# Optimization experiments

Measured on AMD Instinct MI355X. Metric: run time of the kernel, lower is better.

Reference implementation:

```python
import math
import jax, jax.numpy as jnp
import numpy as np

B, S, HID = 1, 2048, 4096
NH, NKV, D = 32, 8, 128
THETA = 10000.0


def setup_inputs() -> dict:
    key = jax.random.key(0)
    k1, k2, k3, k4, k5 = jax.random.split(key, 5)
    hidden_states = jax.random.normal(k1, (B, S, HID), dtype=jnp.float32)
    k_cache = jax.random.normal(k2, (B, NKV, S, D), dtype=jnp.float32)
    v_cache = jax.random.normal(k3, (B, NKV, S, D), dtype=jnp.float32)
    Wq = jax.random.normal(k4, (HID, NH * D), dtype=jnp.float32) * 0.02
    Wo = jax.random.normal(k5, (NH * D, HID), dtype=jnp.float32) * 0.02
    position_ids = jnp.broadcast_to(jnp.arange(S, dtype=jnp.int32), (B, S))
    # causal mask: True = masked out (torch.where(mask, -10000, scores))
    attention_mask = jnp.broadcast_to(
        jnp.triu(jnp.ones((S, S), dtype=bool), k=1)[None, None], (B, 1, S, S)
    )
    return {
        "hidden_states": hidden_states,
        "k_cache": k_cache,
        "v_cache": v_cache,
        "Wq": Wq,
        "Wo": Wo,
        "position_ids": position_ids,
        "attention_mask": attention_mask,
    }


def _rotate_half(x):
    x1, x2 = jnp.split(x, 2, axis=-1)
    return jnp.concatenate([-x2, x1], axis=-1)


def _rope_tables(position_ids):
    # Llama rotary embedding gathered at position_ids -> [B, 1, S, D]
    inv_freq = 1.0 / (THETA ** (jnp.arange(0, D, 2, dtype=jnp.float32) / D))
    freqs = position_ids[..., None].astype(jnp.float32) * inv_freq  # [B, S, D/2]
    emb = jnp.concatenate([freqs, freqs], axis=-1)  # [B, S, D]
    return jnp.cos(emb)[:, None], jnp.sin(emb)[:, None]


def reference(hidden_states, k_cache, v_cache, Wq, Wo, position_ids, attention_mask):
    G = NH // NKV  # GQA group size
    # q projection: [B, S, HID] -> [B, NH, S, D]
    q = (hidden_states @ Wq).reshape(B, S, NH, D).transpose(0, 2, 1, 3)
    cos, sin = _rope_tables(position_ids)
    q = q * cos + _rotate_half(q) * sin
    # GQA without materializing repeat_kv: group query heads over kv heads
    qg = q.reshape(B, NKV, G, S, D)
    scores = jnp.einsum("bkgsd,bktd->bkgst", qg, k_cache) / math.sqrt(D)
    scores = scores.reshape(B, NH, S, S)
    scores = jnp.where(attention_mask, jnp.float32(-10000.0), scores)
    probs = jax.nn.softmax(scores.astype(jnp.float32), axis=-1).astype(q.dtype)
    out = jnp.einsum("bkgst,bktd->bkgsd", probs.reshape(B, NKV, G, S, S), v_cache)
    out = out.reshape(B, NH, S, D).transpose(0, 2, 1, 3).reshape(B, S, NH * D)
    return out @ Wo
```

## Files before the change

### kernel.cpp

```cpp
#include <hip/hip_runtime.h>
#include <cstdint>
#include <cstddef>

#define S_LEN 2048
#define HID 4096
#define NH 32
#define NKV 8
#define HD 128

typedef __attribute__((ext_vector_type(4))) float f32x4;
typedef __attribute__((ext_vector_type(8))) short bf16x8;

__device__ __forceinline__ unsigned short f2bf(float f) {
  union { float f; uint32_t u; } v; v.f = f;
  uint32_t r = v.u + 0x7FFFu + ((v.u >> 16) & 1u);
  return (unsigned short)(r >> 16);
}

__global__ void cvt_bf16_kernel(const float* __restrict__ in,
                                unsigned short* __restrict__ out, int n4) {
  int i = blockIdx.x * blockDim.x + threadIdx.x;
  if (i >= n4) return;
  float4 v = ((const float4*)in)[i];
  ushort4 o;
  o.x = f2bf(v.x); o.y = f2bf(v.y); o.z = f2bf(v.z); o.w = f2bf(v.w);
  ((ushort4*)out)[i] = o;
}

__global__ __launch_bounds__(256) void transpose_cvt2_kernel(
    const float* __restrict__ in0, unsigned short* __restrict__ out0,
    const float* __restrict__ in1, unsigned short* __restrict__ out1,
    int R, int C) {
  __shared__ float tile[64][65];
  const float* inb = (blockIdx.z == 0) ? in0 : in1;
  unsigned short* outb = (blockIdx.z == 0) ? out0 : out1;
  const int c0 = blockIdx.x * 64, r0 = blockIdx.y * 64;
  const int tid = threadIdx.x;
#pragma unroll
  for (int p = 0; p < 4; ++p) {
    const int ch = p * 256 + tid;
    const int r = ch >> 4, off = (ch & 15) << 2;
    *(float4*)&tile[r][off] = *(const float4*)(inb + (size_t)(r0 + r) * C + c0 + off);
  }
  __syncthreads();
#pragma unroll
  for (int p = 0; p < 2; ++p) {
    const int ch = p * 256 + tid;
    const int i = ch >> 3, j0 = (ch & 7) << 3;
    bf16x8 v;
#pragma unroll
    for (int k = 0; k < 8; ++k) v[k] = (short)f2bf(tile[j0 + k][i]);
    *(bf16x8*)(outb + (size_t)(c0 + i) * R + r0 + j0) = v;
  }
}

__global__ __launch_bounds__(256) void transpose_cvt_kernel(
    const float* __restrict__ in, unsigned short* __restrict__ out, int R, int C) {
  __shared__ float tile[64][65];
  const int b = blockIdx.z;
  const float* inb = in + (size_t)b * R * C;
  unsigned short* outb = out + (size_t)b * R * C;
  const int c0 = blockIdx.x * 64, r0 = blockIdx.y * 64;
  const int tid = threadIdx.x;
#pragma unroll
  for (int p = 0; p < 4; ++p) {
    const int ch = p * 256 + tid;
    const int r = ch >> 4, off = (ch & 15) << 2;
    *(float4*)&tile[r][off] = *(const float4*)(inb + (size_t)(r0 + r) * C + c0 + off);
  }
  __syncthreads();
#pragma unroll
  for (int p = 0; p < 2; ++p) {
    const int ch = p * 256 + tid;
    const int i = ch >> 3, j0 = (ch & 7) << 3;
    bf16x8 v;
#pragma unroll
    for (int k = 0; k < 8; ++k) v[k] = (short)f2bf(tile[j0 + k][i]);
    *(bf16x8*)(outb + (size_t)(c0 + i) * R + r0 + j0) = v;
  }
}

__global__ __launch_bounds__(256, 2) void gemm_bt_kernel(
    const unsigned short* __restrict__ A, const unsigned short* __restrict__ BT,
    float* __restrict__ C, int M, int N, int K) {
  __shared__ __align__(16) unsigned short As[128 * 64];
  __shared__ __align__(16) unsigned short Bs[128 * 64];
  const int tid = threadIdx.x;
  const int lane = tid & 63;
  const int wid = tid >> 6;
  const int wm = (wid >> 1) * 64, wn = (wid & 1) * 64;
  const int g = blockIdx.x;
  const int xcd = g & 7, local = g >> 3;
  const int m0 = (xcd * 2 + (local & 1)) * 128;
  const int n0 = (local >> 1) * 128;
  const int lr = lane & 15;
  const int quad = lane >> 4;
  const int sw = lr & 7;
  f32x4 acc[4][4] = {};
  for (int kt = 0; kt < K; kt += 64) {
    __syncthreads();
#pragma unroll
    for (int p = 0; p < 4; ++p) {
      const int c = p * 256 + tid;
      const int r = c >> 3, jsrc = (c & 7) ^ (r & 7);
      __builtin_amdgcn_global_load_lds(
          (const __attribute__((address_space(1))) void*)(A + (size_t)(m0 + r) * K + kt + jsrc * 8),
          (__attribute__((address_space(3))) void*)(As + c * 8), 16, 0, 0);
      __builtin_amdgcn_global_load_lds(
          (const __attribute__((address_space(1))) void*)(BT + (size_t)(n0 + r) * K + kt + jsrc * 8),
          (__attribute__((address_space(3))) void*)(Bs + c * 8), 16, 0, 0);
    }
    __syncthreads();
#pragma unroll
    for (int h = 0; h < 2; ++h) {
      const int pos = ((h * 4 + quad) ^ sw) << 3;
      bf16x8 a[4], b[4];
#pragma unroll
      for (int t = 0; t < 4; ++t) {
        a[t] = *(const bf16x8*)(As + (wm + t * 16 + lr) * 64 + pos);
        b[t] = *(const bf16x8*)(Bs + (wn + t * 16 + lr) * 64 + pos);
      }
#pragma unroll
      for (int mt = 0; mt < 4; ++mt)
#pragma unroll
        for (int nt = 0; nt < 4; ++nt)
          acc[mt][nt] = __builtin_amdgcn_mfma_f32_16x16x32_bf16(a[mt], b[nt], acc[mt][nt], 0, 0, 0);
    }
  }
  const int qd = quad << 2;
#pragma unroll
  for (int mt = 0; mt < 4; ++mt)
#pragma unroll
    for (int nt = 0; nt < 4; ++nt) {
      const int row = m0 + wm + mt * 16 + qd;
      const int col = n0 + wn + nt * 16 + lr;
#pragma unroll
      for (int r = 0; r < 4; ++r)
        C[(size_t)(row + r) * N + col] = acc[mt][nt][r];
    }
}

__global__ __launch_bounds__(256, 2) void gemm_rope_kernel(
    const unsigned short* __restrict__ A, const unsigned short* __restrict__ BT,
    const int* __restrict__ pos_ids, unsigned short* __restrict__ Qout) {
  __shared__ __align__(16) unsigned short As[128 * 64];
  __shared__ __align__(16) unsigned short Bs[128 * 64];
  const int tid = threadIdx.x;
  const int lane = tid & 63;
  const int wid = tid >> 6;
  const int wm = wid * 32;
  const int g = blockIdx.x;
  const int xcd = g & 7, local = g >> 3;
  const int m0 = (xcd * 2 + (local & 1)) * 128;
  const int n0 = (local >> 1) * 128;
  const int lr = lane & 15;
  const int quad = lane >> 4;
  const int sw = lr & 7;
  f32x4 acc[2][8] = {};
  for (int kt = 0; kt < HID; kt += 64) {
    __syncthreads();
#pragma unroll
    for (int p = 0; p < 4; ++p) {
      const int c = p * 256 + tid;
      const int r = c >> 3, jsrc = (c & 7) ^ (r & 7);
      __builtin_amdgcn_global_load_lds(
          (const __attribute__((address_space(1))) void*)(A + (size_t)(m0 + r) * HID + kt + jsrc * 8),
          (__attribute__((address_space(3))) void*)(As + c * 8), 16, 0, 0);
      __builtin_amdgcn_global_load_lds(
          (const __attribute__((address_space(1))) void*)(BT + (size_t)(n0 + r) * HID + kt + jsrc * 8),
          (__attribute__((address_space(3))) void*)(Bs + c * 8), 16, 0, 0);
    }
    __syncthreads();
#pragma unroll
    for (int h = 0; h < 2; ++h) {
      const int pos = ((h * 4 + quad) ^ sw) << 3;
      bf16x8 a[2], b[8];
#pragma unroll
      for (int t = 0; t < 2; ++t)
        a[t] = *(const bf16x8*)(As + (wm + t * 16 + lr) * 64 + pos);
#pragma unroll
      for (int t = 0; t < 8; ++t)
        b[t] = *(const bf16x8*)(Bs + (t * 16 + lr) * 64 + pos);
#pragma unroll
      for (int mt = 0; mt < 2; ++mt)
#pragma unroll
        for (int nt = 0; nt < 8; ++nt)
          acc[mt][nt] = __builtin_amdgcn_mfma_f32_16x16x32_bf16(a[mt], b[nt], acc[mt][nt], 0, 0, 0);
    }
  }
  const int qd = quad << 2;
  const int h = n0 >> 7;
#pragma unroll
  for (int mt = 0; mt < 2; ++mt)
#pragma unroll
    for (int r = 0; r < 4; ++r) {
      const int row = m0 + wm + mt * 16 + qd + r;
      const float pos = (float)pos_ids[row];
#pragma unroll
      for (int nt = 0; nt < 4; ++nt) {
        const int i = nt * 16 + lr;
        const float invf = __expf(-(float)(2 * i) * (9.2103403719761836f / 128.0f));
        float sn, cs;
        __sincosf(pos * invf, &sn, &cs);
        const float x1 = acc[mt][nt][r], x2 = acc[mt][nt + 4][r];
        Qout[((size_t)h * S_LEN + row) * HD + i]      = f2bf(x1 * cs - x2 * sn);
        Qout[((size_t)h * S_LEN + row) * HD + i + 64] = f2bf(x2 * cs + x1 * sn);
      }
    }
}

__global__ __launch_bounds__(256, 2) void attn_kernel(
    const unsigned short* __restrict__ Q, const unsigned short* __restrict__ Kc,
    const unsigned short* __restrict__ VT, unsigned short* __restrict__ Aout) {
  __shared__ __align__(16) unsigned short Ks[64 * 136];
  __shared__ __align__(16) unsigned short Vs[128 * 72];
  __shared__ __align__(16) unsigned short Ps[128 * 72];
  const int tid = threadIdx.x, lane = tid & 63, wid = tid >> 6;
  const int qh = blockIdx.x;
  const int qt = (blockIdx.y < 8) ? (15 - (int)blockIdx.y) : ((int)blockIdx.y - 8);
  const int kvh = qh >> 2;
  const int lr = lane & 15, quad = lane >> 4;
  const float scale = 0.08838834764831843f;

  bf16x8 qf[2][4];
#pragma unroll
  for (int mt = 0; mt < 2; ++mt)
#pragma unroll
    for (int kk = 0; kk < 4; ++kk)
      qf[mt][kk] = *(const bf16x8*)(Q + ((size_t)qh * S_LEN + qt * 128 + wid * 32 + mt * 16 + lr) * HD + kk * 32 + quad * 8);

  f32x4 o[2][8] = {};
  float lsum[2] = {0.f, 0.f};

  const int prow0 = (wid * 32 + lr) * 72;
  const int nkt = 2 * qt + 2;
  for (int kt2 = 0; kt2 < nkt; ++kt2) {
    bf16x8 kr[4], vr[4];
#pragma unroll
    for (int p = 0; p < 4; ++p) {
      const int c = p * 256 + tid;
      kr[p] = *(const bf16x8*)(Kc + ((size_t)kvh * S_LEN + kt2 * 64 + (c >> 4)) * HD + (c & 15) * 8);
      vr[p] = *(const bf16x8*)(VT + ((size_t)kvh * HD + (c >> 3)) * S_LEN + kt2 * 64 + (c & 7) * 8);
    }
    __syncthreads();
#pragma unroll
    for (int p = 0; p < 4; ++p) {
      const int c = p * 256 + tid;
      *(bf16x8*)(Ks + (c >> 4) * 136 + (c & 15) * 8) = kr[p];
      *(bf16x8*)(Vs + (c >> 3) * 72 + (c & 7) * 8) = vr[p];
    }
    __syncthreads();

    const bool dtile = (kt2 >= 2 * qt);
#pragma unroll
    for (int nt = 0; nt < 4; ++nt) {
      f32x4 s0 = {}, s1 = {};
#pragma unroll
      for (int kk = 0; kk < 4; ++kk) {
        bf16x8 kf = *(const bf16x8*)(Ks + (nt * 16 + lr) * 136 + kk * 32 + quad * 8);
        s0 = __builtin_amdgcn_mfma_f32_16x16x32_bf16(kf, qf[0][kk], s0, 0, 0, 0);
        s1 = __builtin_amdgcn_mfma_f32_16x16x32_bf16(kf, qf[1][kk], s1, 0, 0, 0);
      }
      const int skey0 = kt2 * 64 + nt * 16 + quad * 4;
#pragma unroll
      for (int mt = 0; mt < 2; ++mt) {
        const f32x4 s = mt ? s1 : s0;
        const int qrow = qt * 128 + wid * 32 + mt * 16 + lr;
        ushort4 pk;
        float ls = 0.f;
        float pv[4];
#pragma unroll
        for (int r = 0; r < 4; ++r) {
          float v = s[r] * scale - 16.0f;
          if (dtile && (skey0 + r) > qrow) v = -1e30f;
          pv[r] = __expf(v);
          ls += pv[r];
        }
        pk.x = f2bf(pv[0]); pk.y = f2bf(pv[1]); pk.z = f2bf(pv[2]); pk.w = f2bf(pv[3]);
        lsum[mt] += ls;
        *(ushort4*)(Ps + prow0 + mt * 16 * 72 + nt * 16 + quad * 4) = pk;
      }
    }
    bf16x8 pf[2][2];
#pragma unroll
    for (int mt = 0; mt < 2; ++mt)
#pragma unroll
      for (int kk = 0; kk < 2; ++kk)
        pf[mt][kk] = *(const bf16x8*)(Ps + prow0 + mt * 16 * 72 + kk * 32 + quad * 8);
#pragma unroll
    for (int dt = 0; dt < 8; ++dt)
#pragma unroll
      for (int kk = 0; kk < 2; ++kk) {
        bf16x8 vf = *(const bf16x8*)(Vs + (dt * 16 + lr) * 72 + kk * 32 + quad * 8);
        o[0][dt] = __builtin_amdgcn_mfma_f32_16x16x32_bf16(vf, pf[0][kk], o[0][dt], 0, 0, 0);
        o[1][dt] = __builtin_amdgcn_mfma_f32_16x16x32_bf16(vf, pf[1][kk], o[1][dt], 0, 0, 0);
      }
  }

#pragma unroll
  for (int mt = 0; mt < 2; ++mt) {
    float l = lsum[mt];
    l += __shfl_xor(l, 16);
    l += __shfl_xor(l, 32);
    const float inv = 1.0f / l;
    const int qrow = qt * 128 + wid * 32 + mt * 16 + lr;
#pragma unroll
    for (int dt = 0; dt < 8; ++dt) {
      ushort4 w;
      w.x = f2bf(o[mt][dt][0] * inv);
      w.y = f2bf(o[mt][dt][1] * inv);
      w.z = f2bf(o[mt][dt][2] * inv);
      w.w = f2bf(o[mt][dt][3] * inv);
      *(ushort4*)(Aout + (size_t)qrow * HID + qh * HD + dt * 16 + quad * 4) = w;
    }
  }
}

extern "C" void kernel_launch(void* const* d_in, const int* in_sizes, int n_in,
                              void* d_out, int out_size, void* d_ws, size_t ws_size,
                              hipStream_t stream) {
  const float* hidden  = (const float*)d_in[0];
  const float* k_cache = (const float*)d_in[1];
  const float* v_cache = (const float*)d_in[2];
  const float* Wq      = (const float*)d_in[3];
  const float* Wo      = (const float*)d_in[4];
  const int*   pos     = (const int*)d_in[5];
  float* out = (float*)d_out;

  char* ws = (char*)d_ws;
  unsigned short* hidden_bf = (unsigned short*)(ws + 0);
  unsigned short* attn_bf   = hidden_bf;
  unsigned short* WqT       = (unsigned short*)(ws + 16777216);
  unsigned short* WoT       = (unsigned short*)(ws + 50331648);
  unsigned short* k_bf      = (unsigned short*)(ws + 83886080);
  unsigned short* vT        = (unsigned short*)(ws + 88080384);
  unsigned short* q_bf      = (unsigned short*)(ws + 92274688);

  cvt_bf16_kernel<<<(S_LEN * HID / 4 + 255) / 256, 256, 0, stream>>>(hidden, hidden_bf, S_LEN * HID / 4);
  cvt_bf16_kernel<<<(NKV * S_LEN * HD / 4 + 255) / 256, 256, 0, stream>>>(k_cache, k_bf, NKV * S_LEN * HD / 4);
  transpose_cvt2_kernel<<<dim3(HID / 64, HID / 64, 2), 256, 0, stream>>>(Wq, WqT, Wo, WoT, HID, HID);
  transpose_cvt_kernel<<<dim3(HD / 64, S_LEN / 64, NKV), 256, 0, stream>>>(v_cache, vT, S_LEN, HD);

  gemm_rope_kernel<<<dim3((S_LEN / 128) * (HID / 128)), 256, 0, stream>>>(hidden_bf, WqT, pos, q_bf);
  attn_kernel<<<dim3(NH, S_LEN / 128), 256, 0, stream>>>(q_bf, k_bf, vT, attn_bf);
  gemm_bt_kernel<<<dim3((S_LEN / 128) * (HID / 128)), 256, 0, stream>>>(attn_bf, WoT, out, S_LEN, HID, HID);
}
```

Baseline: 421.4 us.

## Merge prep kernels and restructure attention with 8 waves, prefetch, and exp2

Three preprocessing launches (hidden and K conversion plus V transpose) become one prep kernel. The attention kernel now runs 512 threads, with each wave owning 16 query rows instead of 32. It prefetches the next K/V tile into registers while computing on the current one and raises wave priority around the MFMA sections. Softmax switches to exp2 with a folded scale and bias, and bf16 packing uses the hardware packed-convert instruction. More waves per block shorten per-wave work and hide latency, at the cost of reloading the same K/V tiles for smaller per-wave row groups and extra register pressure from the prefetch.

```diff
diff --git a/kernel.cpp b/kernel.cpp
--- a/kernel.cpp
+++ b/kernel.cpp
@@ -10,6 +10,7 @@
 
 typedef __attribute__((ext_vector_type(4))) float f32x4;
 typedef __attribute__((ext_vector_type(8))) short bf16x8;
+typedef __attribute__((ext_vector_type(2))) unsigned int u32x2;
 
 __device__ __forceinline__ unsigned short f2bf(float f) {
   union { float f; uint32_t u; } v; v.f = f;
@@ -17,14 +18,66 @@
   return (unsigned short)(r >> 16);
 }
 
-__global__ void cvt_bf16_kernel(const float* __restrict__ in,
-                                unsigned short* __restrict__ out, int n4) {
-  int i = blockIdx.x * blockDim.x + threadIdx.x;
-  if (i >= n4) return;
-  float4 v = ((const float4*)in)[i];
-  ushort4 o;
-  o.x = f2bf(v.x); o.y = f2bf(v.y); o.z = f2bf(v.z); o.w = f2bf(v.w);
-  ((ushort4*)out)[i] = o;
+__device__ __forceinline__ float exp2_fast(float x) {
+#if __has_builtin(__builtin_amdgcn_exp2f)
+  return __builtin_amdgcn_exp2f(x);
+#else
+  float r; asm("v_exp_f32 %0, %1" : "=v"(r) : "v"(x)); return r;
+#endif
+}
+
+__device__ __forceinline__ unsigned int cvt_pk_bf16(float lo, float hi) {
+  unsigned int r;
+  asm("v_cvt_pk_bf16_f32 %0, %1, %2" : "=v"(r) : "v"(lo), "v"(hi));
+  return r;
+}
+
+__global__ __launch_bounds__(256) void prep_kernel(
+    const float* __restrict__ hidden, unsigned short* __restrict__ hidden_bf,
+    const float* __restrict__ k_cache, unsigned short* __restrict__ k_bf,
+    const float* __restrict__ v_cache, unsigned short* __restrict__ vT) {
+  __shared__ float tile[64][65];
+  const int b = blockIdx.x;
+  const int tid = threadIdx.x;
+  if (b < 8192) {
+    const int i = b * 256 + tid;
+    float4 v = ((const float4*)hidden)[i];
+    ushort4 o;
+    o.x = f2bf(v.x); o.y = f2bf(v.y); o.z = f2bf(v.z); o.w = f2bf(v.w);
+    ((ushort4*)hidden_bf)[i] = o;
+    return;
+  }
+  if (b < 8192 + 2048) {
+    const int i = (b - 8192) * 256 + tid;
+    float4 v = ((const float4*)k_cache)[i];
+    ushort4 o;
+    o.x = f2bf(v.x); o.y = f2bf(v.y); o.z = f2bf(v.z); o.w = f2bf(v.w);
+    ((ushort4*)k_bf)[i] = o;
+    return;
+  }
+  const int bb = b - 10240;
+  const int z = bb >> 6;
+  const int rem = bb & 63;
+  const int c0 = (rem & 1) * 64;
+  const int r0 = (rem >> 1) * 64;
+  const float* inb = v_cache + (size_t)z * S_LEN * HD;
+  unsigned short* outb = vT + (size_t)z * S_LEN * HD;
+#pragma unroll
+  for (int p = 0; p < 4; ++p) {
+    const int ch = p * 256 + tid;
+    const int r = ch >> 4, off = (ch & 15) << 2;
+    *(float4*)&tile[r][off] = *(const float4*)(inb + (size_t)(r0 + r) * HD + c0 + off);
+  }
+  __syncthreads();
+#pragma unroll
+  for (int p = 0; p < 2; ++p) {
+    const int ch = p * 256 + tid;
+    const int i = ch >> 3, j0 = (ch & 7) << 3;
+    bf16x8 v;
+#pragma unroll
+    for (int k = 0; k < 8; ++k) v[k] = (short)f2bf(tile[j0 + k][i]);
+    *(bf16x8*)(outb + (size_t)(c0 + i) * S_LEN + r0 + j0) = v;
+  }
 }
 
 __global__ __launch_bounds__(256) void transpose_cvt2_kernel(
@@ -34,32 +87,6 @@
   __shared__ float tile[64][65];
   const float* inb = (blockIdx.z == 0) ? in0 : in1;
   unsigned short* outb = (blockIdx.z == 0) ? out0 : out1;
-  const int c0 = blockIdx.x * 64, r0 = blockIdx.y * 64;
-  const int tid = threadIdx.x;
-#pragma unroll
-  for (int p = 0; p < 4; ++p) {
-    const int ch = p * 256 + tid;
-    const int r = ch >> 4, off = (ch & 15) << 2;
-    *(float4*)&tile[r][off] = *(const float4*)(inb + (size_t)(r0 + r) * C + c0 + off);
-  }
-  __syncthreads();
-#pragma unroll
-  for (int p = 0; p < 2; ++p) {
-    const int ch = p * 256 + tid;
-    const int i = ch >> 3, j0 = (ch & 7) << 3;
-    bf16x8 v;
-#pragma unroll
-    for (int k = 0; k < 8; ++k) v[k] = (short)f2bf(tile[j0 + k][i]);
-    *(bf16x8*)(outb + (size_t)(c0 + i) * R + r0 + j0) = v;
-  }
-}
-
-__global__ __launch_bounds__(256) void transpose_cvt_kernel(
-    const float* __restrict__ in, unsigned short* __restrict__ out, int R, int C) {
-  __shared__ float tile[64][65];
-  const int b = blockIdx.z;
-  const float* inb = in + (size_t)b * R * C;
-  unsigned short* outb = out + (size_t)b * R * C;
   const int c0 = blockIdx.x * 64, r0 = blockIdx.y * 64;
   const int tid = threadIdx.x;
 #pragma unroll
@@ -209,7 +236,7 @@
     }
 }
 
-__global__ __launch_bounds__(256, 2) void attn_kernel(
+__global__ __launch_bounds__(512, 4) void attn_kernel(
     const unsigned short* __restrict__ Q, const unsigned short* __restrict__ Kc,
     const unsigned short* __restrict__ VT, unsigned short* __restrict__ Aout) {
   __shared__ __align__(16) unsigned short Ks[64 * 136];
@@ -220,99 +247,103 @@
   const int qt = (blockIdx.y < 8) ? (15 - (int)blockIdx.y) : ((int)blockIdx.y - 8);
   const int kvh = qh >> 2;
   const int lr = lane & 15, quad = lane >> 4;
-  const float scale = 0.08838834764831843f;
-
-  bf16x8 qf[2][4];
-#pragma unroll
-  for (int mt = 0; mt < 2; ++mt)
-#pragma unroll
-    for (int kk = 0; kk < 4; ++kk)
-      qf[mt][kk] = *(const bf16x8*)(Q + ((size_t)qh * S_LEN + qt * 128 + wid * 32 + mt * 16 + lr) * HD + kk * 32 + quad * 8);
-
-  f32x4 o[2][8] = {};
-  float lsum[2] = {0.f, 0.f};
-
-  const int prow0 = (wid * 32 + lr) * 72;
+  const float SC = 0.12751619754705767f;
+  const float NB = -23.083120654223414f;
+
+  bf16x8 qf[4];
+#pragma unroll
+  for (int kk = 0; kk < 4; ++kk)
+    qf[kk] = *(const bf16x8*)(Q + ((size_t)qh * S_LEN + qt * 128 + wid * 16 + lr) * HD + kk * 32 + quad * 8);
+
+  f32x4 o[8] = {};
+  float lsum = 0.f;
+  const int prow0 = (wid * 16 + lr) * 72;
+  const int qrow = qt * 128 + wid * 16 + lr;
   const int nkt = 2 * qt + 2;
+
+#pragma unroll
+  for (int p = 0; p < 2; ++p) {
+    const int c = p * 512 + tid;
+    bf16x8 kr0 = *(const bf16x8*)(Kc + ((size_t)kvh * S_LEN + (c >> 4)) * HD + (c & 15) * 8);
+    bf16x8 vr0 = *(const bf16x8*)(VT + ((size_t)kvh * HD + (c >> 3)) * S_LEN + (c & 7) * 8);
+    *(bf16x8*)(Ks + (c >> 4) * 136 + (c & 15) * 8) = kr0;
+    *(bf16x8*)(Vs + (c >> 3) * 72 + (c & 7) * 8) = vr0;
+  }
+  __syncthreads();
+
   for (int kt2 = 0; kt2 < nkt; ++kt2) {
-    bf16x8 kr[4], vr[4];
-#pragma unroll
-    for (int p = 0; p < 4; ++p) {
-      const int c = p * 256 + tid;
-      kr[p] = *(const bf16x8*)(Kc + ((size_t)kvh * S_LEN + kt2 * 64 + (c >> 4)) * HD + (c & 15) * 8);
-      vr[p] = *(const bf16x8*)(VT + ((size_t)kvh * HD + (c >> 3)) * S_LEN + kt2 * 64 + (c & 7) * 8);
-    }
-    __syncthreads();
-#pragma unroll
-    for (int p = 0; p < 4; ++p) {
-      const int c = p * 256 + tid;
-      *(bf16x8*)(Ks + (c >> 4) * 136 + (c & 15) * 8) = kr[p];
-      *(bf16x8*)(Vs + (c >> 3) * 72 + (c & 7) * 8) = vr[p];
-    }
-    __syncthreads();
+    bf16x8 kr[2], vr[2];
+    const bool pref = (kt2 + 1 < nkt);
+    if (pref) {
+#pragma unroll
+      for (int p = 0; p < 2; ++p) {
+        const int c = p * 512 + tid;
+        kr[p] = *(const bf16x8*)(Kc + ((size_t)kvh * S_LEN + (kt2 + 1) * 64 + (c >> 4)) * HD + (c & 15) * 8);
+        vr[p] = *(const bf16x8*)(VT + ((size_t)kvh * HD + (c >> 3)) * S_LEN + (kt2 + 1) * 64 + (c & 7) * 8);
+      }
+    }
 
     const bool dtile = (kt2 >= 2 * qt);
 #pragma unroll
     for (int nt = 0; nt < 4; ++nt) {
-      f32x4 s0 = {}, s1 = {};
+      f32x4 s = {};
+      __builtin_amdgcn_s_setprio(1);
 #pragma unroll
       for (int kk = 0; kk < 4; ++kk) {
         bf16x8 kf = *(const bf16x8*)(Ks + (nt * 16 + lr) * 136 + kk * 32 + quad * 8);
-        s0 = __builtin_amdgcn_mfma_f32_16x16x32_bf16(kf, qf[0][kk], s0, 0, 0, 0);
-        s1 = __builtin_amdgcn_mfma_f32_16x16x32_bf16(kf, qf[1][kk], s1, 0, 0, 0);
-      }
+        s = __builtin_amdgcn_mfma_f32_16x16x32_bf16(kf, qf[kk], s, 0, 0, 0);
+      }
+      __builtin_amdgcn_s_setprio(0);
       const int skey0 = kt2 * 64 + nt * 16 + quad * 4;
-#pragma unroll
-      for (int mt = 0; mt < 2; ++mt) {
-        const f32x4 s = mt ? s1 : s0;
-        const int qrow = qt * 128 + wid * 32 + mt * 16 + lr;
-        ushort4 pk;
-        float ls = 0.f;
-        float pv[4];
-#pragma unroll
-        for (int r = 0; r < 4; ++r) {
-          float v = s[r] * scale - 16.0f;
-          if (dtile && (skey0 + r) > qrow) v = -1e30f;
-          pv[r] = __expf(v);
-          ls += pv[r];
-        }
-        pk.x = f2bf(pv[0]); pk.y = f2bf(pv[1]); pk.z = f2bf(pv[2]); pk.w = f2bf(pv[3]);
-        lsum[mt] += ls;
-        *(ushort4*)(Ps + prow0 + mt * 16 * 72 + nt * 16 + quad * 4) = pk;
-      }
-    }
-    bf16x8 pf[2][2];
-#pragma unroll
-    for (int mt = 0; mt < 2; ++mt)
-#pragma unroll
-      for (int kk = 0; kk < 2; ++kk)
-        pf[mt][kk] = *(const bf16x8*)(Ps + prow0 + mt * 16 * 72 + kk * 32 + quad * 8);
+      float pv[4];
+#pragma unroll
+      for (int r = 0; r < 4; ++r) {
+        float v = fmaf(s[r], SC, NB);
+        if (dtile && (skey0 + r) > qrow) v = -1e30f;
+        pv[r] = exp2_fast(v);
+      }
+      lsum += (pv[0] + pv[1]) + (pv[2] + pv[3]);
+      u32x2 pk;
+      pk.x = cvt_pk_bf16(pv[0], pv[1]);
+      pk.y = cvt_pk_bf16(pv[2], pv[3]);
+      *(u32x2*)(Ps + prow0 + nt * 16 + quad * 4) = pk;
+    }
+    bf16x8 pf[2];
+#pragma unroll
+    for (int kk = 0; kk < 2; ++kk)
+      pf[kk] = *(const bf16x8*)(Ps + prow0 + kk * 32 + quad * 8);
+    __builtin_amdgcn_s_setprio(1);
 #pragma unroll
     for (int dt = 0; dt < 8; ++dt)
 #pragma unroll
       for (int kk = 0; kk < 2; ++kk) {
         bf16x8 vf = *(const bf16x8*)(Vs + (dt * 16 + lr) * 72 + kk * 32 + quad * 8);
-        o[0][dt] = __builtin_amdgcn_mfma_f32_16x16x32_bf16(vf, pf[0][kk], o[0][dt], 0, 0, 0);
-        o[1][dt] = __builtin_amdgcn_mfma_f32_16x16x32_bf16(vf, pf[1][kk], o[1][dt], 0, 0, 0);
-      }
-  }
-
-#pragma unroll
-  for (int mt = 0; mt < 2; ++mt) {
-    float l = lsum[mt];
-    l += __shfl_xor(l, 16);
-    l += __shfl_xor(l, 32);
-    const float inv = 1.0f / l;
-    const int qrow = qt * 128 + wid * 32 + mt * 16 + lr;
-#pragma unroll
-    for (int dt = 0; dt < 8; ++dt) {
-      ushort4 w;
-      w.x = f2bf(o[mt][dt][0] * inv);
-      w.y = f2bf(o[mt][dt][1] * inv);
-      w.z = f2bf(o[mt][dt][2] * inv);
-      w.w = f2bf(o[mt][dt][3] * inv);
-      *(ushort4*)(Aout + (size_t)qrow * HID + qh * HD + dt * 16 + quad * 4) = w;
-    }
+        o[dt] = __builtin_amdgcn_mfma_f32_16x16x32_bf16(vf, pf[kk], o[dt], 0, 0, 0);
+      }
+    __builtin_amdgcn_s_setprio(0);
+
+    if (pref) {
+      __syncthreads();
+#pragma unroll
+      for (int p = 0; p < 2; ++p) {
+        const int c = p * 512 + tid;
+        *(bf16x8*)(Ks + (c >> 4) * 136 + (c & 15) * 8) = kr[p];
+        *(bf16x8*)(Vs + (c >> 3) * 72 + (c & 7) * 8) = vr[p];
+      }
+      __syncthreads();
+    }
+  }
+
+  float l = lsum;
+  l += __shfl_xor(l, 16);
+  l += __shfl_xor(l, 32);
+  const float inv = 1.0f / l;
+#pragma unroll
+  for (int dt = 0; dt < 8; ++dt) {
+    u32x2 w;
+    w.x = cvt_pk_bf16(o[dt][0] * inv, o[dt][1] * inv);
+    w.y = cvt_pk_bf16(o[dt][2] * inv, o[dt][3] * inv);
+    *(u32x2*)(Aout + (size_t)qrow * HID + qh * HD + dt * 16 + quad * 4) = w;
   }
 }
 
@@ -336,12 +367,10 @@
   unsigned short* vT        = (unsigned short*)(ws + 88080384);
   unsigned short* q_bf      = (unsigned short*)(ws + 92274688);
 
-  cvt_bf16_kernel<<<(S_LEN * HID / 4 + 255) / 256, 256, 0, stream>>>(hidden, hidden_bf, S_LEN * HID / 4);
-  cvt_bf16_kernel<<<(NKV * S_LEN * HD / 4 + 255) / 256, 256, 0, stream>>>(k_cache, k_bf, NKV * S_LEN * HD / 4);
+  prep_kernel<<<8192 + 2048 + 512, 256, 0, stream>>>(hidden, hidden_bf, k_cache, k_bf, v_cache, vT);
   transpose_cvt2_kernel<<<dim3(HID / 64, HID / 64, 2), 256, 0, stream>>>(Wq, WqT, Wo, WoT, HID, HID);
-  transpose_cvt_kernel<<<dim3(HD / 64, S_LEN / 64, NKV), 256, 0, stream>>>(v_cache, vT, S_LEN, HD);
 
   gemm_rope_kernel<<<dim3((S_LEN / 128) * (HID / 128)), 256, 0, stream>>>(hidden_bf, WqT, pos, q_bf);
-  attn_kernel<<<dim3(NH, S_LEN / 128), 256, 0, stream>>>(q_bf, k_bf, vT, attn_bf);
+  attn_kernel<<<dim3(NH, S_LEN / 128), 512, 0, stream>>>(q_bf, k_bf, vT, attn_bf);
   gemm_bt_kernel<<<dim3((S_LEN / 128) * (HID / 128)), 256, 0, stream>>>(attn_bf, WoT, out, S_LEN, HID, HID);
 }
```

Measured after the change: 442.4 us. 5.0% more time.
